# Performance work log

Hardware: AMD Instinct MI355X
Metric: run time of the kernel (lower is better)

## Reference

```python
import jax, jax.numpy as jnp
import numpy as np

B, L, D, H = 4, 2048, 1024, 16
HD = D // H


def setup_inputs() -> dict:
    key = jax.random.key(0)
    ks = jax.random.split(key, 12)
    s = 1.0 / np.sqrt(D)
    return {
        "q": jax.random.normal(ks[0], (B, L, D), jnp.float32),
        "k": jax.random.normal(ks[1], (B, L, D), jnp.float32),
        "v": jax.random.normal(ks[2], (B, L, D), jnp.float32),
        "mask": jax.random.randint(ks[3], (1, 1, L, L), 0, 2, jnp.int32),
        "Wq": jax.random.normal(ks[4], (D, D), jnp.float32) * s,
        "bq": jnp.zeros((D,), jnp.float32),
        "Wk": jax.random.normal(ks[5], (D, D), jnp.float32) * s,
        "bk": jnp.zeros((D,), jnp.float32),
        "Wv": jax.random.normal(ks[6], (D, D), jnp.float32) * s,
        "bv": jnp.zeros((D,), jnp.float32),
        "Wo": jax.random.normal(ks[7], (D, D), jnp.float32) * s,
        "bo": jnp.zeros((D,), jnp.float32),
    }


def _split_heads(x):
    # (B, L, D) -> (B, H, L, HD)
    b, l, _ = x.shape
    return x.reshape(b, l, H, HD).transpose(0, 2, 1, 3)


def reference(q, k, v, mask, Wq, bq, Wk, bk, Wv, bv, Wo, bo):
    qw = q @ Wq.T + bq
    kw = k @ Wk.T + bk
    vw = v @ Wv.T + bv
    qh, kh, vh = _split_heads(qw), _split_heads(kw), _split_heads(vw)
    scale = 1.0 / jnp.sqrt(jnp.float32(HD))
    scores = jnp.einsum('bhqd,bhkd->bhqk', qh, kh) * scale
    scores = scores + mask.astype(scores.dtype) * (-1e15)
    weights = jax.nn.softmax(scores, axis=-1)
    attn = jnp.einsum('bhqk,bhkd->bhqd', weights, vh)  # (B, H, L, HD)
    attn = attn.transpose(0, 2, 1, 3).reshape(q.shape[0], q.shape[1], D)
    return attn @ Wo.T + bo
```

## Files before the change

kernel.cpp:

```cpp
#include <hip/hip_runtime.h>
#include <stdint.h>

#define B_ 4
#define L_ 2048
#define D_ 1024
#define H_ 16
#define HD_ 64

typedef __attribute__((ext_vector_type(8))) short short8;
typedef __attribute__((ext_vector_type(4))) float f32x4;

__device__ __forceinline__ unsigned short f2bf(float f) {
  union { float f; unsigned int u; } x; x.f = f;
  unsigned int u = x.u;
  u += 0x7FFFu + ((u >> 16) & 1u);
  return (unsigned short)(u >> 16);
}

__device__ __forceinline__ f32x4 zero4() {
  f32x4 z; z[0] = 0.f; z[1] = 0.f; z[2] = 0.f; z[3] = 0.f; return z;
}

__device__ __forceinline__ void gload_lds16(const unsigned short* gp, unsigned short* lp) {
  __builtin_amdgcn_global_load_lds(
      (const __attribute__((address_space(1))) unsigned int*)(const void*)gp,
      (__attribute__((address_space(3))) unsigned int*)(void*)lp, 16, 0, 0);
}

__global__ __launch_bounds__(256) void cast4_bf16(
    const float* __restrict__ s0, const float* __restrict__ s1,
    const float* __restrict__ s2, const float* __restrict__ s3,
    unsigned short* __restrict__ d0, unsigned short* __restrict__ d1,
    unsigned short* __restrict__ d2, unsigned short* __restrict__ d3, int n) {
  int w = blockIdx.y;
  const float* src = (w == 0) ? s0 : (w == 1) ? s1 : (w == 2) ? s2 : s3;
  unsigned short* dst = (w == 0) ? d0 : (w == 1) ? d1 : (w == 2) ? d2 : d3;
  int stride = gridDim.x * blockDim.x * 4;
  for (int i = (blockIdx.x * blockDim.x + threadIdx.x) * 4; i < n; i += stride) {
    float4 f = *(const float4*)(src + i);
    uint2 o;
    o.x = (unsigned int)f2bf(f.x) | ((unsigned int)f2bf(f.y) << 16);
    o.y = (unsigned int)f2bf(f.z) | ((unsigned int)f2bf(f.w) << 16);
    *(uint2*)(dst + i) = o;
  }
}

__global__ __launch_bounds__(256) void mask_pack2(const int* __restrict__ m,
                                                  unsigned long long* __restrict__ words) {
  int wid = blockIdx.x * 4 + (threadIdx.x >> 6);
  int lane = threadIdx.x & 63;
  int qt = wid >> 5, kt = wid & 31;
  int q = qt * 16 + (lane & 15);
  int g = lane >> 4;
  #pragma unroll
  for (int w = 0; w < 16; ++w) {
    int nt = w >> 2, r = w & 3;
    int key = kt * 64 + nt * 16 + g * 4 + r;
    unsigned long long bal = __ballot(m[(size_t)q * L_ + key] != 0);
    if (lane == 0) words[((size_t)qt * 32 + kt) * 16 + w] = bal;
  }
}

template<int MODE, int ASTAGE, bool FUSE2>
__global__ __launch_bounds__(256) void gemm_bt(
    const void* __restrict__ A0v, const void* __restrict__ A1v,
    const unsigned short* __restrict__ B0w, const unsigned short* __restrict__ B1w,
    const float* __restrict__ bias0, const float* __restrict__ bias1,
    void* __restrict__ C0p, void* __restrict__ C1p,
    float scale0, float scale1, int K)
{
  __shared__ __align__(16) unsigned short As[128 * 64];
  __shared__ __align__(16) unsigned short Bs[128 * 64];
  __shared__ __align__(16) unsigned short Tsh[MODE == 2 ? 64 * 136 : 16];
  const int t = threadIdx.x;
  const int lane = t & 63;
  const int wave = t >> 6;
  const int g = lane >> 4, cl = lane & 15;
  const int wm = wave >> 1, wn = wave & 1;

  const int bx = blockIdx.x;
  const int by = blockIdx.y;
  const int bz = FUSE2 ? blockIdx.z : 0;

  const void* Av = (FUSE2 && bz) ? A1v : A0v;
  const unsigned short* Bw = (FUSE2 && bz) ? B1w : B0w;
  const float* bias = (FUSE2 && bz) ? bias1 : bias0;
  void* Cp = (FUSE2 && bz) ? C1p : C0p;
  const float scale = (FUSE2 && bz) ? scale1 : scale0;

  const int m0 = bx * 128, n0 = by * 128;

  f32x4 acc[4][4];
  #pragma unroll
  for (int i = 0; i < 4; ++i)
    #pragma unroll
    for (int j = 0; j < 4; ++j) acc[i][j] = zero4();

  for (int k0 = 0; k0 < K; k0 += 64) {
    __syncthreads();
    #pragma unroll
    for (int i = 0; i < 4; ++i) {
      int c = i * 256 + t;
      int row = c >> 3, cc = c & 7;
      int scc = ((cc ^ (row & 7)) << 3);
      if constexpr (ASTAGE == 1) {
        const float* Af = (const float*)Av;
        const float* ap = Af + (size_t)(m0 + row) * K + k0 + cc * 8;
        float4 f0 = *(const float4*)ap;
        float4 f1 = *(const float4*)(ap + 4);
        unsigned int u0, u1, u2, u3;
        asm("v_cvt_pk_bf16_f32 %0, %1, %2" : "=v"(u0) : "v"(f0.x), "v"(f0.y));
        asm("v_cvt_pk_bf16_f32 %0, %1, %2" : "=v"(u1) : "v"(f0.z), "v"(f0.w));
        asm("v_cvt_pk_bf16_f32 %0, %1, %2" : "=v"(u2) : "v"(f1.x), "v"(f1.y));
        asm("v_cvt_pk_bf16_f32 %0, %1, %2" : "=v"(u3) : "v"(f1.z), "v"(f1.w));
        uint4 u; u.x = u0; u.y = u1; u.z = u2; u.w = u3;
        *(uint4*)&As[row * 64 + scc] = u;
      } else if constexpr (ASTAGE == 2) {
        const unsigned short* ap = (const unsigned short*)Av
                                   + (size_t)(m0 + row) * K + k0 + cc * 8;
        short8 av = *(const short8*)ap;
        *(short8*)&As[row * 64 + scc] = av;
      } else {
        gload_lds16((const unsigned short*)Av + (size_t)(m0 + row) * K + k0 + scc,
                    &As[c << 3]);
      }
      gload_lds16(Bw + (size_t)(n0 + row) * K + k0 + scc, &Bs[c << 3]);
    }
    __syncthreads();
    #pragma unroll
    for (int kk = 0; kk < 2; ++kk) {
      short8 af[4], bf[4];
      #pragma unroll
      for (int mt = 0; mt < 4; ++mt)
        af[mt] = *(const short8*)&As[(wm * 64 + mt * 16 + cl) * 64
                                     + ((kk * 32 + g * 8) ^ ((cl & 7) << 3))];
      #pragma unroll
      for (int nt = 0; nt < 4; ++nt)
        bf[nt] = *(const short8*)&Bs[(wn * 64 + nt * 16 + cl) * 64
                                     + ((kk * 32 + g * 8) ^ ((cl & 7) << 3))];
      #pragma unroll
      for (int mt = 0; mt < 4; ++mt)
        #pragma unroll
        for (int nt = 0; nt < 4; ++nt)
          acc[mt][nt] = __builtin_amdgcn_mfma_f32_16x16x32_bf16(af[mt], bf[nt], acc[mt][nt], 0, 0, 0);
    }
  }

  if constexpr (MODE <= 1) {
    #pragma unroll
    for (int nt = 0; nt < 4; ++nt) {
      int col = n0 + wn * 64 + nt * 16 + cl;
      float bv = bias[col];
      #pragma unroll
      for (int mt = 0; mt < 4; ++mt) {
        #pragma unroll
        for (int r = 0; r < 4; ++r) {
          int row = m0 + wm * 64 + mt * 16 + g * 4 + r;
          float val = (acc[mt][nt][r] + bv) * scale;
          if (MODE == 0)
            ((float*)Cp)[(size_t)row * D_ + col] = val;
          else
            ((unsigned short*)Cp)[(size_t)row * D_ + col] = f2bf(val);
        }
      }
    }
  } else {
    const int b = m0 >> 11;
    #pragma unroll 1
    for (int half = 0; half < 2; ++half) {
      __syncthreads();
      if (wn == half) {
        #pragma unroll
        for (int nt = 0; nt < 4; ++nt) {
          float bv = bias[n0 + wn * 64 + nt * 16 + cl];
          #pragma unroll
          for (int mt = 0; mt < 4; ++mt) {
            float v0 = acc[mt][nt][0] + bv, v1 = acc[mt][nt][1] + bv;
            float v2 = acc[mt][nt][2] + bv, v3 = acc[mt][nt][3] + bv;
            unsigned int lo, hi;
            asm("v_cvt_pk_bf16_f32 %0, %1, %2" : "=v"(lo) : "v"(v0), "v"(v1));
            asm("v_cvt_pk_bf16_f32 %0, %1, %2" : "=v"(hi) : "v"(v2), "v"(v3));
            uint2 u; u.x = lo; u.y = hi;
            *(uint2*)&Tsh[(nt * 16 + cl) * 136 + wm * 64 + mt * 16 + g * 4] = u;
          }
        }
      }
      __syncthreads();
      #pragma unroll
      for (int p = 0; p < 4; ++p) {
        int chunk = p * 256 + t;
        int c = chunk >> 4, li = (chunk & 15) * 8;
        int colg = n0 + half * 64 + c;
        int hh = colg >> 6, d = colg & 63;
        short8 vv = *(const short8*)&Tsh[c * 136 + li];
        *(short8*)((unsigned short*)Cp + (((size_t)(b * 16 + hh)) << 17)
                   + (size_t)d * L_ + (m0 & (L_ - 1)) + li) = vv;
      }
    }
  }
}

__global__ __launch_bounds__(256) void flash_attn(
    const unsigned short* __restrict__ qw,
    const unsigned short* __restrict__ kw,
    const unsigned short* __restrict__ vt,
    const unsigned long long* __restrict__ mwords,
    unsigned short* __restrict__ ctx)
{
  __shared__ __align__(16) unsigned short Ksh[2][64 * 64];
  __shared__ __align__(16) unsigned short Vsh[2][64 * 64];
  __shared__ __align__(16) unsigned short Psh[64 * 64];

  const int t = threadIdx.x;
  const int lane = t & 63;
  const int wave = t >> 6;
  const int g = lane >> 4, cl = lane & 15;

  const int d0i = blockIdx.x;
  const int xq = (d0i >> 3) & 31;
  const int bh = (d0i & 7) + ((d0i >> 8) << 3);
  const int b = bh >> 4, h = bh & 15;
  const int qb = xq * 64 + wave * 16;

  const size_t baseq = (size_t)b * L_ * D_ + (size_t)h * HD_;
  const size_t basev = (size_t)bh * HD_ * L_;

  const int qtu = __builtin_amdgcn_readfirstlane(xq * 4 + wave);
  const unsigned long long* __restrict__ mrow = mwords + (size_t)qtu * (32 * 16);

  const int c0 = t, c1 = 256 + t;
  const int r0 = c0 >> 3, r1 = c1 >> 3;
  const int s0 = ((c0 & 7) ^ (r0 & 7)) << 3, s1 = ((c1 & 7) ^ (r1 & 7)) << 3;
  const unsigned short* kg0 = kw + baseq + (size_t)r0 * D_ + s0;
  const unsigned short* kg1 = kw + baseq + (size_t)r1 * D_ + s1;
  const unsigned short* vg0 = vt + basev + (size_t)r0 * L_ + s0;
  const unsigned short* vg1 = vt + basev + (size_t)r1 * L_ + s1;

#define STAGE_KV(bufi, kti)                                                     \
  {                                                                             \
    const size_t ko = (size_t)(kti) * (64 * D_);                                \
    const int vo = (kti) * 64;                                                  \
    gload_lds16(kg0 + ko, &Ksh[bufi][c0 << 3]);                                 \
    gload_lds16(vg0 + vo, &Vsh[bufi][c0 << 3]);                                 \
    gload_lds16(kg1 + ko, &Ksh[bufi][c1 << 3]);                                 \
    gload_lds16(vg1 + vo, &Vsh[bufi][c1 << 3]);                                 \
  }

  short8 bq[2];
  #pragma unroll
  for (int kk = 0; kk < 2; ++kk)
    bq[kk] = *(const short8*)(qw + baseq + (size_t)(qb + cl) * D_ + kk * 32 + g * 8);

  short8 ones;
  #pragma unroll
  for (int i = 0; i < 8; ++i) ones[i] = (short)0x3F80;

  f32x4 oacc[4], lsum;
  #pragma unroll
  for (int dt = 0; dt < 4; ++dt) oacc[dt] = zero4();
  lsum = zero4();
  float ninf = -1e30f;

  STAGE_KV(0, 0);
  __syncthreads();

  int buf = 0;
  for (int kt = 0; kt < L_ / 64; ++kt) {
    unsigned long long Mw[16];
    #pragma unroll
    for (int w = 0; w < 16; ++w) Mw[w] = mrow[kt * 16 + w];

    if (kt + 1 < L_ / 64) STAGE_KV(buf ^ 1, kt + 1);

    f32x4 sc[4];
    #pragma unroll
    for (int nt = 0; nt < 4; ++nt) {
      sc[nt][0] = -16.f; sc[nt][1] = -16.f; sc[nt][2] = -16.f; sc[nt][3] = -16.f;
    }
    __builtin_amdgcn_s_setprio(1);
    #pragma unroll
    for (int kk = 0; kk < 2; ++kk) {
      #pragma unroll
      for (int nt = 0; nt < 4; ++nt) {
        short8 ak = *(const short8*)&Ksh[buf][(nt * 16 + cl) * 64
                                             + ((kk * 32 + g * 8) ^ ((cl & 7) << 3))];
        sc[nt] = __builtin_amdgcn_mfma_f32_16x16x32_bf16(ak, bq[kk], sc[nt], 0, 0, 0);
      }
    }
    __builtin_amdgcn_s_setprio(0);

    float p[4][4];
    #pragma unroll
    for (int nt = 0; nt < 4; ++nt)
      #pragma unroll
      for (int r = 0; r < 4; ++r) {
        float sv;
        asm("v_cndmask_b32 %0, %1, %2, %3"
            : "=v"(sv)
            : "v"(sc[nt][r]), "v"(ninf), "s"(Mw[nt * 4 + r]));
        p[nt][r] = __builtin_amdgcn_exp2f(sv);
      }

    #pragma unroll
    for (int nt = 0; nt < 4; ++nt) {
      unsigned int lo, hi;
      asm("v_cvt_pk_bf16_f32 %0, %1, %2" : "=v"(lo) : "v"(p[nt][0]), "v"(p[nt][1]));
      asm("v_cvt_pk_bf16_f32 %0, %1, %2" : "=v"(hi) : "v"(p[nt][2]), "v"(p[nt][3]));
      uint2 u; u.x = lo; u.y = hi;
      *(uint2*)&Psh[(((wave * 16 + cl) * 64) + nt * 16 + g * 4) ^ ((cl & 7) << 3)] = u;
    }

    short8 pa[2];
    #pragma unroll
    for (int kk = 0; kk < 2; ++kk)
      pa[kk] = *(const short8*)&Psh[(((wave * 16 + cl) * 64) + kk * 32 + g * 8)
                                    ^ ((cl & 7) << 3)];
    __builtin_amdgcn_s_setprio(1);
    #pragma unroll
    for (int kk = 0; kk < 2; ++kk) {
      #pragma unroll
      for (int dt = 0; dt < 4; ++dt) {
        short8 bv = *(const short8*)&Vsh[buf][(dt * 16 + cl) * 64
                                             + ((kk * 32 + g * 8) ^ ((cl & 7) << 3))];
        oacc[dt] = __builtin_amdgcn_mfma_f32_16x16x32_bf16(pa[kk], bv, oacc[dt], 0, 0, 0);
      }
      lsum = __builtin_amdgcn_mfma_f32_16x16x32_bf16(pa[kk], ones, lsum, 0, 0, 0);
    }
    __builtin_amdgcn_s_setprio(0);

    __syncthreads();
    buf ^= 1;
  }

  #pragma unroll
  for (int r = 0; r < 4; ++r) {
    float iv = __builtin_amdgcn_rcpf(lsum[r]);
    #pragma unroll
    for (int dt = 0; dt < 4; ++dt)
      ctx[baseq + (size_t)(qb + g * 4 + r) * D_ + dt * 16 + cl] = f2bf(oacc[dt][r] * iv);
  }
#undef STAGE_KV
}

extern "C" void kernel_launch(void* const* d_in, const int* in_sizes, int n_in,
                              void* d_out, int out_size, void* d_ws, size_t ws_size,
                              hipStream_t stream) {
  (void)in_sizes; (void)n_in; (void)out_size; (void)ws_size;
  const float* q    = (const float*)d_in[0];
  const float* k    = (const float*)d_in[1];
  const float* v    = (const float*)d_in[2];
  const int*   mask = (const int*)d_in[3];
  const float* Wq   = (const float*)d_in[4];
  const float* bq   = (const float*)d_in[5];
  const float* Wk   = (const float*)d_in[6];
  const float* bk   = (const float*)d_in[7];
  const float* Wv   = (const float*)d_in[8];
  const float* bv   = (const float*)d_in[9];
  const float* Wo   = (const float*)d_in[10];
  const float* bo   = (const float*)d_in[11];

  char* ws = (char*)d_ws;
  const size_t MB = 1024 * 1024;
  unsigned short* Wqb  = (unsigned short*)(ws + 16 * MB);
  unsigned short* Wkb  = (unsigned short*)(ws + 18 * MB);
  unsigned short* Wvb  = (unsigned short*)(ws + 20 * MB);
  unsigned short* Wob  = (unsigned short*)(ws + 22 * MB);
  unsigned short* qwb  = (unsigned short*)(ws + 24 * MB);
  unsigned short* kwb  = (unsigned short*)(ws + 40 * MB);
  unsigned short* vtb  = (unsigned short*)(ws + 56 * MB);
  unsigned short* ctx  = (unsigned short*)(ws + 72 * MB);
  unsigned long long* mwd = (unsigned long long*)(ws + 88 * MB);

  const int NW = D_ * D_;

  cast4_bf16<<<dim3(512, 4), 256, 0, stream>>>(Wq, Wk, Wv, Wo, Wqb, Wkb, Wvb, Wob, NW);
  mask_pack2<<<1024, 256, 0, stream>>>(mask, mwd);

  dim3 gproj(64, 8);
  dim3 gproj2(64, 8, 2);

  const float QSCALE = 0.125f * 1.44269504088896340736f;

  gemm_bt<1, 1, true><<<gproj2, 256, 0, stream>>>(
      q, k, Wqb, Wkb, bq, bk, qwb, kwb, QSCALE, 1.0f, D_);
  gemm_bt<2, 1, false><<<gproj, 256, 0, stream>>>(
      v, v, Wvb, Wvb, bv, bv, vtb, vtb, 1.0f, 1.0f, D_);

  flash_attn<<<dim3(2048), 256, 0, stream>>>(qwb, kwb, vtb, mwd, ctx);

  gemm_bt<0, 2, false><<<gproj, 256, 0, stream>>>(
      ctx, ctx, Wob, Wob, bo, bo, d_out, d_out, 1.0f, 1.0f, D_);
}
```

Baseline: 238.7 us.

## Add dedicated 64x128-tile bf16 GEMM kernel for output projection

Replaces the generic gemm_bt launch for the output projection with a new kernel built on 64x128 tiles and 128-thread blocks. The grid grows from 512 to 1024 blocks to spread the M=8192 by N=1024 GEMM across more CUs. It prefetches A through registers and loads B into XOR-swizzled LDS using global_load_lds. Smaller tiles cut per-block data reuse, and the output writes are scattered 4-byte fp32 stores that may coalesce worse than the original epilogue.

```diff
diff --git a/kernel.cpp b/kernel.cpp
--- a/kernel.cpp
+++ b/kernel.cpp
@@ -200,6 +200,89 @@
   }
 }
 
+__global__ __launch_bounds__(128) void gemm_out64(
+    const unsigned short* __restrict__ A,
+    const unsigned short* __restrict__ Bw,
+    const float* __restrict__ bias,
+    float* __restrict__ Cp, int K)
+{
+  __shared__ __align__(16) unsigned short As[64 * 64];
+  __shared__ __align__(16) unsigned short Bs[128 * 64];
+  const int t = threadIdx.x;
+  const int lane = t & 63;
+  const int wn = t >> 6;
+  const int g = lane >> 4, cl = lane & 15;
+  const int m0 = blockIdx.x * 64, n0 = blockIdx.y * 128;
+
+  f32x4 acc[4][4];
+  #pragma unroll
+  for (int i = 0; i < 4; ++i)
+    #pragma unroll
+    for (int j = 0; j < 4; ++j) acc[i][j] = zero4();
+
+  short8 apf[4];
+  #pragma unroll
+  for (int i = 0; i < 4; ++i) {
+    int c = i * 128 + t; int row = c >> 3, cc = c & 7;
+    apf[i] = *(const short8*)(A + (size_t)(m0 + row) * K + cc * 8);
+  }
+
+  for (int k0 = 0; k0 < K; k0 += 64) {
+    __syncthreads();
+    #pragma unroll
+    for (int i = 0; i < 4; ++i) {
+      int c = i * 128 + t; int row = c >> 3, cc = c & 7;
+      int scc = ((cc ^ (row & 7)) << 3);
+      *(short8*)&As[row * 64 + scc] = apf[i];
+    }
+    #pragma unroll
+    for (int i = 0; i < 8; ++i) {
+      int c = i * 128 + t; int row = c >> 3, cc = c & 7;
+      int scc = ((cc ^ (row & 7)) << 3);
+      gload_lds16(Bw + (size_t)(n0 + row) * K + k0 + scc, &Bs[c << 3]);
+    }
+    __syncthreads();
+    if (k0 + 64 < K) {
+      #pragma unroll
+      for (int i = 0; i < 4; ++i) {
+        int c = i * 128 + t; int row = c >> 3, cc = c & 7;
+        apf[i] = *(const short8*)(A + (size_t)(m0 + row) * K + k0 + 64 + cc * 8);
+      }
+    }
+    #pragma unroll
+    for (int kk = 0; kk < 2; ++kk) {
+      short8 af[4], bf[4];
+      #pragma unroll
+      for (int mt = 0; mt < 4; ++mt)
+        af[mt] = *(const short8*)&As[(mt * 16 + cl) * 64
+                                     + ((kk * 32 + g * 8) ^ ((cl & 7) << 3))];
+      #pragma unroll
+      for (int nt = 0; nt < 4; ++nt)
+        bf[nt] = *(const short8*)&Bs[(wn * 64 + nt * 16 + cl) * 64
+                                     + ((kk * 32 + g * 8) ^ ((cl & 7) << 3))];
+      #pragma unroll
+      for (int mt = 0; mt < 4; ++mt)
+        #pragma unroll
+        for (int nt = 0; nt < 4; ++nt)
+          acc[mt][nt] = __builtin_amdgcn_mfma_f32_16x16x32_bf16(af[mt], bf[nt], acc[mt][nt], 0, 0, 0);
+    }
+  }
+
+  #pragma unroll
+  for (int nt = 0; nt < 4; ++nt) {
+    int col = n0 + wn * 64 + nt * 16 + cl;
+    float bv = bias[col];
+    #pragma unroll
+    for (int mt = 0; mt < 4; ++mt) {
+      #pragma unroll
+      for (int r = 0; r < 4; ++r) {
+        int row = m0 + mt * 16 + g * 4 + r;
+        Cp[(size_t)row * D_ + col] = acc[mt][nt][r] + bv;
+      }
+    }
+  }
+}
+
 __global__ __launch_bounds__(256) void flash_attn(
     const unsigned short* __restrict__ qw,
     const unsigned short* __restrict__ kw,
@@ -388,6 +471,5 @@
 
   flash_attn<<<dim3(2048), 256, 0, stream>>>(qwb, kwb, vtb, mwd, ctx);
 
-  gemm_bt<0, 2, false><<<gproj, 256, 0, stream>>>(
-      ctx, ctx, Wob, Wob, bo, bo, d_out, d_out, 1.0f, 1.0f, D_);
-}
+  gemm_out64<<<dim3(128, 8), 128, 0, stream>>>(ctx, Wob, bo, (float*)d_out, D_);
+}
```

Result: no change. 239.5 us (+0.4%).
